# Kernel optimization log

Hardware: AMD Instinct MI355X
Metric: run time of the kernel (lower is better)

Reference implementation:

```python
import jax, jax.numpy as jnp
import numpy as np

N_NODES = 100000
N_EDGES = 1600000
IN_FEATS, HIDDEN_FEATS, OUT_FEATS = 32, 64, 16


def setup_inputs() -> dict:
    key = jax.random.key(0)
    ks = jax.random.split(key, 8)
    return {
        "features": jax.random.normal(ks[0], (N_NODES, IN_FEATS), dtype=jnp.float32),
        "src": jax.random.randint(ks[1], (N_EDGES,), 0, N_NODES, dtype=jnp.int64),
        "dst": jax.random.randint(ks[2], (N_EDGES,), 0, N_NODES, dtype=jnp.int64),
        "W1_self": jax.random.normal(ks[3], (IN_FEATS, HIDDEN_FEATS), dtype=jnp.float32) * 0.1,
        "W1_neigh": jax.random.normal(ks[4], (IN_FEATS, HIDDEN_FEATS), dtype=jnp.float32) * 0.1,
        "b1": jnp.zeros((HIDDEN_FEATS,), dtype=jnp.float32),
        "W2_self": jax.random.normal(ks[5], (HIDDEN_FEATS, OUT_FEATS), dtype=jnp.float32) * 0.1,
        "W2_neigh": jax.random.normal(ks[6], (HIDDEN_FEATS, OUT_FEATS), dtype=jnp.float32) * 0.1,
        "b2": jnp.zeros((OUT_FEATS,), dtype=jnp.float32),
    }


def _sage_conv_mean(h, src, dst, n_nodes, W_self, W_neigh, b):
    # DGL SAGEConv(mean): gather src features to edges, mean-reduce at dst,
    # then fc_self(h) + fc_neigh(mean_neigh) + bias.
    ones = jnp.ones(src.shape, dtype=h.dtype)
    deg = jax.ops.segment_sum(ones, dst, num_segments=n_nodes)  # in-degree [N]
    agg = jax.ops.segment_sum(h[src], dst, num_segments=n_nodes)  # [N, d]
    mean_neigh = agg / jnp.maximum(deg, 1.0)[:, None]
    return h @ W_self + mean_neigh @ W_neigh + b


def reference(features, src, dst, W1_self, W1_neigh, b1, W2_self, W2_neigh, b2):
    n = features.shape[0]
    h = _sage_conv_mean(features, src, dst, n, W1_self, W1_neigh, b1)
    h = jax.nn.relu(h)
    # dropout is identity at inference (Keras call default training=False)
    out = _sage_conv_mean(h, src, dst, n, W2_self, W2_neigh, b2)
    return out
```

## Files before the change

kernel.cpp:

```cpp
#include <hip/hip_runtime.h>

#define N_NODES 100000
#define N_EDGES 1600000
#define IN_F 32
#define HID_F 64
#define OUT_F 16
#define BSIZE 512
#define NBKT 256
#define CAP 10240
#define CHUNK 4096
#define NBUCK ((N_NODES + BSIZE - 1) / BSIZE)
#define NCHUNK ((N_EDGES + CHUNK - 1) / CHUNK)
#define CAPN 48
#define APITCH 68

using f2v = __attribute__((ext_vector_type(2))) float;

#define ADDQ(s, Q) do { f2v p_; \
  p_ = __builtin_amdgcn_cvt_pk_f32_fp8((int)(Q).x, false); s[0] += p_[0]; s[1] += p_[1]; \
  p_ = __builtin_amdgcn_cvt_pk_f32_fp8((int)(Q).x, true);  s[2] += p_[0]; s[3] += p_[1]; \
  p_ = __builtin_amdgcn_cvt_pk_f32_fp8((int)(Q).y, false); s[4] += p_[0]; s[5] += p_[1]; \
  p_ = __builtin_amdgcn_cvt_pk_f32_fp8((int)(Q).y, true);  s[6] += p_[0]; s[7] += p_[1]; \
  p_ = __builtin_amdgcn_cvt_pk_f32_fp8((int)(Q).z, false); s[8] += p_[0]; s[9] += p_[1]; \
  p_ = __builtin_amdgcn_cvt_pk_f32_fp8((int)(Q).z, true);  s[10] += p_[0]; s[11] += p_[1]; \
  p_ = __builtin_amdgcn_cvt_pk_f32_fp8((int)(Q).w, false); s[12] += p_[0]; s[13] += p_[1]; \
  p_ = __builtin_amdgcn_cvt_pk_f32_fp8((int)(Q).w, true);  s[14] += p_[0]; s[15] += p_[1]; \
} while (0)

__global__ __launch_bounds__(NBKT) void cursor_init_kernel(int* __restrict__ cursor) {
  cursor[threadIdx.x] = threadIdx.x * CAP;
}

__global__ __launch_bounds__(512) void bucket_kernel(
    const int* __restrict__ src, const int* __restrict__ dst,
    const float4* __restrict__ featin, uint4* __restrict__ featfp8,
    int* __restrict__ cursor, unsigned* __restrict__ sorted) {
  __shared__ unsigned stage[CHUNK];
  __shared__ unsigned char sbkt[CHUNK];
  __shared__ int lcnt[NBKT], lscan[NBKT], goff[NBKT];
  __shared__ int wsum[4];
  int t = threadIdx.x;

  {
    int gtid = blockIdx.x * 512 + t;
    if (gtid < N_NODES * IN_F / 16) {
      float4 a = featin[4 * gtid], bb = featin[4 * gtid + 1];
      float4 c4 = featin[4 * gtid + 2], d = featin[4 * gtid + 3];
      uint4 r;
      int w;
      w = __builtin_amdgcn_cvt_pk_fp8_f32(a.x, a.y, 0, false);
      w = __builtin_amdgcn_cvt_pk_fp8_f32(a.z, a.w, w, true);
      r.x = (unsigned)w;
      w = __builtin_amdgcn_cvt_pk_fp8_f32(bb.x, bb.y, 0, false);
      w = __builtin_amdgcn_cvt_pk_fp8_f32(bb.z, bb.w, w, true);
      r.y = (unsigned)w;
      w = __builtin_amdgcn_cvt_pk_fp8_f32(c4.x, c4.y, 0, false);
      w = __builtin_amdgcn_cvt_pk_fp8_f32(c4.z, c4.w, w, true);
      r.z = (unsigned)w;
      w = __builtin_amdgcn_cvt_pk_fp8_f32(d.x, d.y, 0, false);
      w = __builtin_amdgcn_cvt_pk_fp8_f32(d.z, d.w, w, true);
      r.w = (unsigned)w;
      featfp8[gtid] = r;
    }
  }

  if (t < NBKT) lcnt[t] = 0;
  __syncthreads();

  int base = blockIdx.x * CHUNK;
  unsigned mypk[CHUNK / 512];
  int myb[CHUNK / 512], myrank[CHUNK / 512];
#pragma unroll
  for (int i = 0; i < CHUNK / 512; ++i) {
    int e = base + t + 512 * i;
    if (e < N_EDGES) {
      unsigned s = (unsigned)src[e], d = (unsigned)dst[e];
      myb[i] = (int)(d >> 9);
      mypk[i] = (s << 9) | (d & 511u);
      myrank[i] = atomicAdd(&lcnt[myb[i]], 1);
    } else {
      myb[i] = -1;
    }
  }
  __syncthreads();

  int x = 0;
  if (t < NBKT) {
    x = lcnt[t];
#pragma unroll
    for (int off = 1; off < 64; off <<= 1) {
      int y = __shfl_up(x, off);
      if ((t & 63) >= off) x += y;
    }
    if ((t & 63) == 63) wsum[t >> 6] = x;
  }
  __syncthreads();
  if (t < NBKT) {
    int w = t >> 6, add = 0;
    if (w > 0) add += wsum[0];
    if (w > 1) add += wsum[1];
    if (w > 2) add += wsum[2];
    int incl = x + add;
    lscan[t] = incl;
    int gb = lcnt[t] ? atomicAdd(&cursor[t], lcnt[t]) : 0;
    goff[t] = gb - incl + lcnt[t];
  }
  __syncthreads();

#pragma unroll
  for (int i = 0; i < CHUNK / 512; ++i) {
    if (myb[i] >= 0) {
      int slot = (lscan[myb[i]] - lcnt[myb[i]]) + myrank[i];
      stage[slot] = mypk[i];
      sbkt[slot] = (unsigned char)myb[i];
    }
  }
  __syncthreads();
  int nvalid = min(CHUNK, N_EDGES - base);
  for (int i = t; i < nvalid; i += 512) {
    int b = (int)sbkt[i];
    sorted[goff[b] + i] = stage[i];
  }
}

__global__ __launch_bounds__(1024) void csr_kernel(
    const unsigned* __restrict__ sorted, const int* __restrict__ cursor,
    int* __restrict__ cnt, int* __restrict__ col) {
  __shared__ int dcnt[BSIZE];
  int t = threadIdx.x;
  int b = blockIdx.x;
  if (t < BSIZE) dcnt[t] = 0;
  __syncthreads();

  int cbase = b * CAP;
  int ne = cursor[b] - cbase;
  const uint4* S4 = (const uint4*)(sorted + cbase);
  int nv4 = ne >> 2;
  for (int i = t; i < nv4; i += 1024) {
    uint4 pp = S4[i];
    int d0 = (int)(pp.x & (BSIZE - 1)), r0 = atomicAdd(&dcnt[d0], 1);
    int d1 = (int)(pp.y & (BSIZE - 1)), r1 = atomicAdd(&dcnt[d1], 1);
    int d2 = (int)(pp.z & (BSIZE - 1)), r2 = atomicAdd(&dcnt[d2], 1);
    int d3 = (int)(pp.w & (BSIZE - 1)), r3 = atomicAdd(&dcnt[d3], 1);
    if (r0 < CAPN) col[(b * BSIZE + d0) * CAPN + r0] = (int)(pp.x >> 9);
    if (r1 < CAPN) col[(b * BSIZE + d1) * CAPN + r1] = (int)(pp.y >> 9);
    if (r2 < CAPN) col[(b * BSIZE + d2) * CAPN + r2] = (int)(pp.z >> 9);
    if (r3 < CAPN) col[(b * BSIZE + d3) * CAPN + r3] = (int)(pp.w >> 9);
  }
  {
    int rem = ne & 3;
    if (t < rem) {
      unsigned p = sorted[cbase + (nv4 << 2) + t];
      int d = (int)(p & (BSIZE - 1));
      int r = atomicAdd(&dcnt[d], 1);
      if (r < CAPN) col[(b * BSIZE + d) * CAPN + r] = (int)(p >> 9);
    }
  }
  __syncthreads();
  if (t < BSIZE) {
    int v = b * BSIZE + t;
    if (v < N_NODES) cnt[v] = dcnt[t];
  }
}

__global__ __launch_bounds__(256) void l1g_kernel(
    const float* __restrict__ feat, const uint4* __restrict__ featfp8,
    const int* __restrict__ cnt, const int* __restrict__ col,
    const float* __restrict__ W1s, const float* __restrict__ W1n,
    const float* __restrict__ b1,
    const float* __restrict__ W2n, const float* __restrict__ W2s,
    unsigned* __restrict__ t2f8, float* __restrict__ s2) {
  __shared__ float sA[64 * APITCH];
  __shared__ float sW[64 * 64];

  int t = threadIdx.x;
  int tile = blockIdx.x * 64;
  int nvalid = min(64, N_NODES - tile);

  const float4* Fg = (const float4*)(feat + (size_t)tile * IN_F);
  int lim = nvalid * 8;
  int fi0 = t, fi1 = t + 256;
  float4 fa0, fa1;
  if (fi0 < lim) fa0 = Fg[fi0];
  if (fi1 < lim) fa1 = Fg[fi1];
  float4 wv[4];
#pragma unroll
  for (int it = 0; it < 4; ++it) {
    int idx = t + 256 * it;
    int row = idx >> 4;
    const float4* srcw = (row < 32) ? (const float4*)W1s : (const float4*)W1n;
    wv[it] = srcw[(row & 31) * 16 + (idx & 15)];
  }

  {
    int nl = t >> 2, c = (t >> 1) & 1, hp = t & 1;
    int v = tile + nl;
    if (nl < nvalid) {
      int deg = cnt[v];
      int start = v * CAPN;
      int dclamp = min(deg, CAPN);
      int end = start + dclamp;
      float s[16];
#pragma unroll
      for (int j = 0; j < 16; ++j) s[j] = 0.0f;
      int nf = dclamp & ~7;
      for (int g = 0; g < nf; g += 8) {
        int4 cc = *(const int4*)&col[start + g + 4 * hp];
        uint4 q0 = featfp8[cc.x * 2 + c];
        uint4 q1 = featfp8[cc.y * 2 + c];
        uint4 q2 = featfp8[cc.z * 2 + c];
        uint4 q3 = featfp8[cc.w * 2 + c];
        ADDQ(s, q0);
        ADDQ(s, q1);
        ADDQ(s, q2);
        ADDQ(s, q3);
      }
      for (int e = start + nf + hp; e < end; e += 2) {
        uint4 q = featfp8[col[e] * 2 + c];
        ADDQ(s, q);
      }
#pragma unroll
      for (int j = 0; j < 16; ++j) s[j] += __shfl_xor(s[j], 1);
      float inv = 1.0f / fmaxf((float)deg, 1.0f);
      int j0 = 8 * hp;
#pragma unroll
      for (int j = 0; j < 8; ++j)
        sA[(32 + 16 * c + j0 + j) * APITCH + nl] = s[j0 + j] * inv;
    }
  }

  if (fi0 < lim) {
    int n = fi0 >> 3, c8 = fi0 & 7;
    sA[(4 * c8 + 0) * APITCH + n] = fa0.x;
    sA[(4 * c8 + 1) * APITCH + n] = fa0.y;
    sA[(4 * c8 + 2) * APITCH + n] = fa0.z;
    sA[(4 * c8 + 3) * APITCH + n] = fa0.w;
  }
  if (fi1 < lim) {
    int n = fi1 >> 3, c8 = fi1 & 7;
    sA[(4 * c8 + 0) * APITCH + n] = fa1.x;
    sA[(4 * c8 + 1) * APITCH + n] = fa1.y;
    sA[(4 * c8 + 2) * APITCH + n] = fa1.z;
    sA[(4 * c8 + 3) * APITCH + n] = fa1.w;
  }
  {
    float4* Ws = (float4*)sW;
#pragma unroll
    for (int it = 0; it < 4; ++it) Ws[t + 256 * it] = wv[it];
  }

  int tx = t & 15, ty = t >> 4;
  int n0 = 4 * ty, c0 = 4 * tx;
  float4 bb = ((const float4*)b1)[tx];
  __syncthreads();

  float acc[4][4];
#pragma unroll
  for (int i = 0; i < 4; ++i) { acc[i][0] = bb.x; acc[i][1] = bb.y; acc[i][2] = bb.z; acc[i][3] = bb.w; }
#pragma unroll 4
  for (int k = 0; k < 64; ++k) {
    float4 a = *(const float4*)&sA[k * APITCH + n0];
    float4 w = *(const float4*)&sW[k * 64 + c0];
    acc[0][0] += a.x * w.x; acc[0][1] += a.x * w.y; acc[0][2] += a.x * w.z; acc[0][3] += a.x * w.w;
    acc[1][0] += a.y * w.x; acc[1][1] += a.y * w.y; acc[1][2] += a.y * w.z; acc[1][3] += a.y * w.w;
    acc[2][0] += a.z * w.x; acc[2][1] += a.z * w.y; acc[2][2] += a.z * w.z; acc[2][3] += a.z * w.w;
    acc[3][0] += a.w * w.x; acc[3][1] += a.w * w.y; acc[3][2] += a.w * w.z; acc[3][3] += a.w * w.w;
  }
  __syncthreads();

#pragma unroll
  for (int jj = 0; jj < 4; ++jj) {
    float4 v;
    v.x = fmaxf(acc[0][jj], 0.0f);
    v.y = fmaxf(acc[1][jj], 0.0f);
    v.z = fmaxf(acc[2][jj], 0.0f);
    v.w = fmaxf(acc[3][jj], 0.0f);
    *(float4*)&sA[(c0 + jj) * APITCH + n0] = v;
  }
  {
    float4* Ws = (float4*)sW;
#pragma unroll
    for (int it = 0; it < 2; ++it) {
      int idx = t + 256 * it;
      int row = idx >> 3, ch = idx & 7;
      const float4* srcw = (ch < 4) ? (const float4*)W2n : (const float4*)W2s;
      Ws[row * 8 + ch] = srcw[row * 4 + (ch & 3)];
    }
  }
  __syncthreads();

  int c2 = 2 * tx;
  float a0 = 0.f, a1 = 0.f, b0 = 0.f, b1_ = 0.f, d0 = 0.f, d1 = 0.f, e0 = 0.f, e1 = 0.f;
#pragma unroll 4
  for (int k = 0; k < 64; ++k) {
    float4 a = *(const float4*)&sA[k * APITCH + n0];
    float2 w = *(const float2*)&sW[k * 32 + c2];
    a0 += a.x * w.x; a1 += a.x * w.y;
    b0 += a.y * w.x; b1_ += a.y * w.y;
    d0 += a.z * w.x; d1 += a.z * w.y;
    e0 += a.w * w.x; e1 += a.w * w.y;
  }
  {
    float rs[4][2] = {{a0, a1}, {b0, b1_}, {d0, d1}, {e0, e1}};
    int cc = c2 & 15;
#pragma unroll
    for (int i = 0; i < 4; ++i) {
      int v = tile + n0 + i;
      if (v < N_NODES) {
        if (c2 < 16) {
          int w = __builtin_amdgcn_cvt_pk_fp8_f32(rs[i][0], rs[i][1], 0, false);
          *(unsigned short*)((char*)t2f8 + (size_t)v * 16 + cc) = (unsigned short)w;
        } else {
          *(float2*)&s2[v * OUT_F + cc] = make_float2(rs[i][0], rs[i][1]);
        }
      }
    }
  }
}

__global__ __launch_bounds__(256) void gather2_final_kernel(
    const int* __restrict__ cnt, const int* __restrict__ col,
    const uint4* __restrict__ t2f8, const float* __restrict__ s2,
    const float* __restrict__ b2, float* __restrict__ out) {
  int g = blockIdx.x * 256 + threadIdx.x;
  int v = g >> 1, hp = g & 1;
  if (v >= N_NODES) return;
  int deg = cnt[v];
  int start = v * CAPN;
  int dclamp = min(deg, CAPN);
  int end = start + dclamp;
  float s[16];
#pragma unroll
  for (int j = 0; j < 16; ++j) s[j] = 0.0f;
  int nf = dclamp & ~7;
  for (int gg = 0; gg < nf; gg += 8) {
    int4 cc = *(const int4*)&col[start + gg + 4 * hp];
    uint4 q0 = t2f8[cc.x];
    uint4 q1 = t2f8[cc.y];
    uint4 q2 = t2f8[cc.z];
    uint4 q3 = t2f8[cc.w];
    ADDQ(s, q0);
    ADDQ(s, q1);
    ADDQ(s, q2);
    ADDQ(s, q3);
  }
  for (int e = start + nf + hp; e < end; e += 2) {
    uint4 q = t2f8[col[e]];
    ADDQ(s, q);
  }
#pragma unroll
  for (int j = 0; j < 16; ++j) s[j] += __shfl_xor(s[j], 1);
  float inv = 1.0f / fmaxf((float)deg, 1.0f);
  const float4* S = (const float4*)s2;
  const float4* B = (const float4*)b2;
  float4* O = (float4*)out;
#pragma unroll
  for (int i = 0; i < 2; ++i) {
    int ii = 2 * hp + i;
    float4 sv = S[v * 4 + ii];
    float4 bv = B[ii];
    float4 r;
    r.x = sv.x + bv.x + s[4 * ii + 0] * inv;
    r.y = sv.y + bv.y + s[4 * ii + 1] * inv;
    r.z = sv.z + bv.z + s[4 * ii + 2] * inv;
    r.w = sv.w + bv.w + s[4 * ii + 3] * inv;
    O[v * 4 + ii] = r;
  }
}

extern "C" void kernel_launch(void* const* d_in, const int* in_sizes, int n_in,
                              void* d_out, int out_size, void* d_ws, size_t ws_size,
                              hipStream_t stream) {
  const float* feat = (const float*)d_in[0];
  const int* src    = (const int*)d_in[1];
  const int* dst    = (const int*)d_in[2];
  const float* W1s  = (const float*)d_in[3];
  const float* W1n  = (const float*)d_in[4];
  const float* b1   = (const float*)d_in[5];
  const float* W2s  = (const float*)d_in[6];
  const float* W2n  = (const float*)d_in[7];
  const float* b2   = (const float*)d_in[8];
  float* out = (float*)d_out;

  const size_t N = N_NODES;
  const size_t SLAB = (size_t)NBUCK * CAP;
  int* cnt = (int*)d_ws;
  int* col = cnt + N + 16;
  unsigned* sorted = (unsigned*)(col + N * CAPN + 16);
  float* s2 = (float*)sorted;
  unsigned* featfp8 = (unsigned*)(sorted + SLAB + 16);
  unsigned* t2f8 = featfp8 + 8 * N;
  int* cursor = (int*)(t2f8 + 4 * N);

  cursor_init_kernel<<<1, NBKT, 0, stream>>>(cursor);
  bucket_kernel<<<NCHUNK, 512, 0, stream>>>(
      src, dst, (const float4*)feat, (uint4*)featfp8, cursor, sorted);
  csr_kernel<<<NBUCK, 1024, 0, stream>>>(sorted, cursor, cnt, col);
  l1g_kernel<<<(N_NODES + 63) / 64, 256, 0, stream>>>(
      feat, (const uint4*)featfp8, cnt, col, W1s, W1n, b1, W2n, W2s, t2f8, s2);
  gather2_final_kernel<<<(2 * N_NODES + 255) / 256, 256, 0, stream>>>(
      cnt, col, (const uint4*)t2f8, s2, b2, out);
}
```

Measured before the change: 163.4 us.

## Split layer-1 GEMM into column halves and use 4 threads per node in gather2

The layer-1 tile GEMM now runs in two passes over 32-column halves of the weight matrix. This halves the sW shared buffer and the per-thread accumulators, and launch bounds are set to 6 blocks to raise occupancy. The cost is an extra weight reload and extra barriers. Separately, the layer-2 gather now uses four lanes per node instead of two, with a second shuffle reduction, for more memory-level parallelism, at the price of more threads and redundant per-node loads.

```diff
diff --git a/kernel.cpp b/kernel.cpp
--- a/kernel.cpp
+++ b/kernel.cpp
@@ -163,7 +163,7 @@
   }
 }
 
-__global__ __launch_bounds__(256) void l1g_kernel(
+__global__ __launch_bounds__(256, 6) void l1g_kernel(
     const float* __restrict__ feat, const uint4* __restrict__ featfp8,
     const int* __restrict__ cnt, const int* __restrict__ col,
     const float* __restrict__ W1s, const float* __restrict__ W1n,
@@ -171,7 +171,7 @@
     const float* __restrict__ W2n, const float* __restrict__ W2s,
     unsigned* __restrict__ t2f8, float* __restrict__ s2) {
   __shared__ float sA[64 * APITCH];
-  __shared__ float sW[64 * 64];
+  __shared__ float sW[64 * 32];
 
   int t = threadIdx.x;
   int tile = blockIdx.x * 64;
@@ -183,13 +183,14 @@
   float4 fa0, fa1;
   if (fi0 < lim) fa0 = Fg[fi0];
   if (fi1 < lim) fa1 = Fg[fi1];
-  float4 wv[4];
-#pragma unroll
-  for (int it = 0; it < 4; ++it) {
+  float4 wa[2], wb[2];
+#pragma unroll
+  for (int it = 0; it < 2; ++it) {
     int idx = t + 256 * it;
-    int row = idx >> 4;
+    int row = idx >> 3, q = idx & 7;
     const float4* srcw = (row < 32) ? (const float4*)W1s : (const float4*)W1n;
-    wv[it] = srcw[(row & 31) * 16 + (idx & 15)];
+    wa[it] = srcw[(row & 31) * 16 + q];
+    wb[it] = srcw[(row & 31) * 16 + 8 + q];
   }
 
   {
@@ -246,36 +247,63 @@
   {
     float4* Ws = (float4*)sW;
 #pragma unroll
-    for (int it = 0; it < 4; ++it) Ws[t + 256 * it] = wv[it];
+    for (int it = 0; it < 2; ++it) Ws[t + 256 * it] = wa[it];
   }
 
   int tx = t & 15, ty = t >> 4;
-  int n0 = 4 * ty, c0 = 4 * tx;
-  float4 bb = ((const float4*)b1)[tx];
-  __syncthreads();
-
-  float acc[4][4];
-#pragma unroll
-  for (int i = 0; i < 4; ++i) { acc[i][0] = bb.x; acc[i][1] = bb.y; acc[i][2] = bb.z; acc[i][3] = bb.w; }
+  int n0 = 4 * ty, cA = 2 * tx;
+  float2 bbA = ((const float2*)b1)[tx];
+  float2 bbB = ((const float2*)b1)[16 + tx];
+  __syncthreads();
+
+  float aA[4][2], aB[4][2];
+#pragma unroll
+  for (int i = 0; i < 4; ++i) {
+    aA[i][0] = bbA.x; aA[i][1] = bbA.y;
+    aB[i][0] = bbB.x; aB[i][1] = bbB.y;
+  }
 #pragma unroll 4
   for (int k = 0; k < 64; ++k) {
     float4 a = *(const float4*)&sA[k * APITCH + n0];
-    float4 w = *(const float4*)&sW[k * 64 + c0];
-    acc[0][0] += a.x * w.x; acc[0][1] += a.x * w.y; acc[0][2] += a.x * w.z; acc[0][3] += a.x * w.w;
-    acc[1][0] += a.y * w.x; acc[1][1] += a.y * w.y; acc[1][2] += a.y * w.z; acc[1][3] += a.y * w.w;
-    acc[2][0] += a.z * w.x; acc[2][1] += a.z * w.y; acc[2][2] += a.z * w.z; acc[2][3] += a.z * w.w;
-    acc[3][0] += a.w * w.x; acc[3][1] += a.w * w.y; acc[3][2] += a.w * w.z; acc[3][3] += a.w * w.w;
-  }
-  __syncthreads();
-
-#pragma unroll
-  for (int jj = 0; jj < 4; ++jj) {
+    float2 w = *(const float2*)&sW[k * 32 + cA];
+    aA[0][0] += a.x * w.x; aA[0][1] += a.x * w.y;
+    aA[1][0] += a.y * w.x; aA[1][1] += a.y * w.y;
+    aA[2][0] += a.z * w.x; aA[2][1] += a.z * w.y;
+    aA[3][0] += a.w * w.x; aA[3][1] += a.w * w.y;
+  }
+  __syncthreads();
+  {
+    float4* Ws = (float4*)sW;
+#pragma unroll
+    for (int it = 0; it < 2; ++it) Ws[t + 256 * it] = wb[it];
+  }
+  __syncthreads();
+
+#pragma unroll 4
+  for (int k = 0; k < 64; ++k) {
+    float4 a = *(const float4*)&sA[k * APITCH + n0];
+    float2 w = *(const float2*)&sW[k * 32 + cA];
+    aB[0][0] += a.x * w.x; aB[0][1] += a.x * w.y;
+    aB[1][0] += a.y * w.x; aB[1][1] += a.y * w.y;
+    aB[2][0] += a.z * w.x; aB[2][1] += a.z * w.y;
+    aB[3][0] += a.w * w.x; aB[3][1] += a.w * w.y;
+  }
+  __syncthreads();
+
+#pragma unroll
+  for (int j = 0; j < 2; ++j) {
     float4 v;
-    v.x = fmaxf(acc[0][jj], 0.0f);
-    v.y = fmaxf(acc[1][jj], 0.0f);
-    v.z = fmaxf(acc[2][jj], 0.0f);
-    v.w = fmaxf(acc[3][jj], 0.0f);
-    *(float4*)&sA[(c0 + jj) * APITCH + n0] = v;
+    v.x = fmaxf(aA[0][j], 0.0f);
+    v.y = fmaxf(aA[1][j], 0.0f);
+    v.z = fmaxf(aA[2][j], 0.0f);
+    v.w = fmaxf(aA[3][j], 0.0f);
+    *(float4*)&sA[(cA + j) * APITCH + n0] = v;
+    float4 u;
+    u.x = fmaxf(aB[0][j], 0.0f);
+    u.y = fmaxf(aB[1][j], 0.0f);
+    u.z = fmaxf(aB[2][j], 0.0f);
+    u.w = fmaxf(aB[3][j], 0.0f);
+    *(float4*)&sA[(32 + cA + j) * APITCH + n0] = u;
   }
   {
     float4* Ws = (float4*)sW;
@@ -289,7 +317,7 @@
   }
   __syncthreads();
 
-  int c2 = 2 * tx;
+  int c2 = cA;
   float a0 = 0.f, a1 = 0.f, b0 = 0.f, b1_ = 0.f, d0 = 0.f, d1 = 0.f, e0 = 0.f, e1 = 0.f;
 #pragma unroll 4
   for (int k = 0; k < 64; ++k) {
@@ -323,7 +351,7 @@
     const uint4* __restrict__ t2f8, const float* __restrict__ s2,
     const float* __restrict__ b2, float* __restrict__ out) {
   int g = blockIdx.x * 256 + threadIdx.x;
-  int v = g >> 1, hp = g & 1;
+  int v = g >> 2, hp = g & 3;
   if (v >= N_NODES) return;
   int deg = cnt[v];
   int start = v * CAPN;
@@ -332,8 +360,8 @@
   float s[16];
 #pragma unroll
   for (int j = 0; j < 16; ++j) s[j] = 0.0f;
-  int nf = dclamp & ~7;
-  for (int gg = 0; gg < nf; gg += 8) {
+  int nf = dclamp & ~15;
+  for (int gg = 0; gg < nf; gg += 16) {
     int4 cc = *(const int4*)&col[start + gg + 4 * hp];
     uint4 q0 = t2f8[cc.x];
     uint4 q1 = t2f8[cc.y];
@@ -344,28 +372,36 @@
     ADDQ(s, q2);
     ADDQ(s, q3);
   }
-  for (int e = start + nf + hp; e < end; e += 2) {
+  int e0 = start + nf;
+  if (dclamp - nf >= 8) {
+    int2 cc = *(const int2*)&col[e0 + 2 * hp];
+    uint4 q0 = t2f8[cc.x];
+    uint4 q1 = t2f8[cc.y];
+    ADDQ(s, q0);
+    ADDQ(s, q1);
+    e0 += 8;
+  }
+  for (int e = e0 + hp; e < end; e += 4) {
     uint4 q = t2f8[col[e]];
     ADDQ(s, q);
   }
 #pragma unroll
   for (int j = 0; j < 16; ++j) s[j] += __shfl_xor(s[j], 1);
+#pragma unroll
+  for (int j = 0; j < 16; ++j) s[j] += __shfl_xor(s[j], 2);
   float inv = 1.0f / fmaxf((float)deg, 1.0f);
-  const float4* S = (const float4*)s2;
-  const float4* B = (const float4*)b2;
-  float4* O = (float4*)out;
-#pragma unroll
-  for (int i = 0; i < 2; ++i) {
-    int ii = 2 * hp + i;
-    float4 sv = S[v * 4 + ii];
-    float4 bv = B[ii];
-    float4 r;
-    r.x = sv.x + bv.x + s[4 * ii + 0] * inv;
-    r.y = sv.y + bv.y + s[4 * ii + 1] * inv;
-    r.z = sv.z + bv.z + s[4 * ii + 2] * inv;
-    r.w = sv.w + bv.w + s[4 * ii + 3] * inv;
-    O[v * 4 + ii] = r;
-  }
+  float q0 = (hp == 0) ? s[0]  : (hp == 1) ? s[4]  : (hp == 2) ? s[8]  : s[12];
+  float q1 = (hp == 0) ? s[1]  : (hp == 1) ? s[5]  : (hp == 2) ? s[9]  : s[13];
+  float q2 = (hp == 0) ? s[2]  : (hp == 1) ? s[6]  : (hp == 2) ? s[10] : s[14];
+  float q3 = (hp == 0) ? s[3]  : (hp == 1) ? s[7]  : (hp == 2) ? s[11] : s[15];
+  float4 sv = ((const float4*)s2)[v * 4 + hp];
+  float4 bv = ((const float4*)b2)[hp];
+  float4 r;
+  r.x = sv.x + bv.x + q0 * inv;
+  r.y = sv.y + bv.y + q1 * inv;
+  r.z = sv.z + bv.z + q2 * inv;
+  r.w = sv.w + bv.w + q3 * inv;
+  ((float4*)out)[v * 4 + hp] = r;
 }
 
 extern "C" void kernel_launch(void* const* d_in, const int* in_sizes, int n_in,
@@ -398,6 +434,6 @@
   csr_kernel<<<NBUCK, 1024, 0, stream>>>(sorted, cursor, cnt, col);
   l1g_kernel<<<(N_NODES + 63) / 64, 256, 0, stream>>>(
       feat, (const uint4*)featfp8, cnt, col, W1s, W1n, b1, W2n, W2s, t2f8, s2);
-  gather2_final_kernel<<<(2 * N_NODES + 255) / 256, 256, 0, stream>>>(
+  gather2_final_kernel<<<(4 * N_NODES + 255) / 256, 256, 0, stream>>>(
       cnt, col, (const uint4*)t2f8, s2, b2, out);
 }
```

Result: slower. 188.8 us (+15.5%).
